# Optimization experiments

Measured on AMD Instinct MI355X. Metric: run time of the kernel, lower is better.

## Reference

```python
import math
import jax, jax.numpy as jnp
import numpy as np

L, H, D, FF, V, S = 12, 12, 768, 3072, 32000, 1024
HD = D // H
EPS = 1e-5
B, T = 2, 1024


def layernorm(x, w, b):
    mu = jnp.mean(x, axis=-1, keepdims=True)
    var = jnp.mean(jnp.square(x - mu), axis=-1, keepdims=True)
    return (x - mu) * jax.lax.rsqrt(var + EPS) * w + b


def setup_inputs() -> dict:
    key = jax.random.key(0)
    ks = jax.random.split(key, 12)
    std = 0.02
    std_res = 0.02 / math.sqrt(2 * L)  # out_proj / down_proj scaled init
    return {
        "input_ids": jax.random.randint(ks[0], (B, T), 0, V),
        "tok_emb": jax.random.normal(ks[1], (V, D), jnp.float32) * std,
        "pos_emb": jax.random.normal(ks[2], (S, D), jnp.float32) * std,
        "ln1_w": jnp.ones((L, D), jnp.float32),
        "ln1_b": jnp.zeros((L, D), jnp.float32),
        "qkv_w": jax.random.normal(ks[3], (L, 3 * D, D), jnp.float32) * std,
        "out_w": jax.random.normal(ks[4], (L, D, D), jnp.float32) * std_res,
        "ln2_w": jnp.ones((L, D), jnp.float32),
        "ln2_b": jnp.zeros((L, D), jnp.float32),
        "up_w": jax.random.normal(ks[5], (L, FF, D), jnp.float32) * std,
        "down_w": jax.random.normal(ks[6], (L, D, FF), jnp.float32) * std_res,
        "lnf_w": jnp.ones((D,), jnp.float32),
        "lnf_b": jnp.zeros((D,), jnp.float32),
    }


def reference(input_ids, tok_emb, pos_emb, ln1_w, ln1_b, qkv_w, out_w,
              ln2_w, ln2_b, up_w, down_w, lnf_w, lnf_b):
    b, t = input_ids.shape
    x = tok_emb[input_ids] + pos_emb[:t]  # (B,T,D); dropout = eval no-op
    causal = jnp.tril(jnp.ones((t, t), bool))  # (T,T)
    scale = 1.0 / math.sqrt(HD)

    def block(x, p):
        l1w, l1b, qkvw, ow, l2w, l2b, uw, dw = p
        h = layernorm(x, l1w, l1b)
        qkv = h @ qkvw.T  # (B,T,3D)
        q, k, v = jnp.split(qkv, 3, axis=-1)
        q = q.reshape(b, t, H, HD)
        k = k.reshape(b, t, H, HD)
        v = v.reshape(b, t, H, HD)
        scores = jnp.einsum('bihd,bjhd->bhij', q, k) * scale
        scores = jnp.where(causal, scores, -jnp.inf)
        probs = jax.nn.softmax(scores, axis=-1)  # attn_dropout = eval no-op
        o = jnp.einsum('bhij,bjhd->bihd', probs, v).reshape(b, t, D)
        x = x + o @ ow.T
        h2 = layernorm(x, l2w, l2b)
        x = x + jax.nn.gelu(h2 @ uw.T, approximate=False) @ dw.T
        return x, None

    x, _ = jax.lax.scan(block, x, (ln1_w, ln1_b, qkv_w, out_w, ln2_w, ln2_b, up_w, down_w))
    x = layernorm(x, lnf_w, lnf_b)
    logits = x @ tok_emb.T  # tied lm_head
    return logits
```

## Files before the change

### kernel.cpp

```cpp
#include <hip/hip_runtime.h>
#include <hip/hip_bf16.h>
#include <math.h>

#define L_  12
#define H_  12
#define D_  768
#define FF_ 3072
#define V_  32000
#define T_  1024
#define B_  2
#define BT_ (B_*T_)

typedef unsigned short ushort_t;
typedef unsigned int   uint_t;
typedef __bf16 bf16x8 __attribute__((ext_vector_type(8)));
typedef float  f32x4  __attribute__((ext_vector_type(4)));

__device__ __forceinline__ uint_t f2bf1(float f) {
    uint_t u = __builtin_bit_cast(uint_t, f);
    return (u + 0x7FFFu + ((u >> 16) & 1u)) >> 16;
}
__device__ __forceinline__ uint_t f2bf2(float lo, float hi) {
    return f2bf1(lo) | (f2bf1(hi) << 16);
}

__device__ __forceinline__ void gl_lds16(const ushort_t* g, ushort_t* l) {
    __builtin_amdgcn_global_load_lds(
        (const __attribute__((address_space(1))) uint_t*)g,
        (__attribute__((address_space(3))) uint_t*)l, 16, 0, 0);
}

__global__ __launch_bounds__(256) void cast_bf16(const float* __restrict__ in,
                                                 ushort_t* __restrict__ out, int n8)
{
    for (int i = blockIdx.x * 256 + threadIdx.x; i < n8; i += gridDim.x * 256) {
        const float4* p = (const float4*)(in + (size_t)i * 8);
        float4 a = p[0], b = p[1];
        *(uint4*)(out + (size_t)i * 8) =
            make_uint4(f2bf2(a.x,a.y), f2bf2(a.z,a.w), f2bf2(b.x,b.y), f2bf2(b.z,b.w));
    }
}

__global__ __launch_bounds__(256) void cast_layer(const float* __restrict__ q,
    const float* __restrict__ o, const float* __restrict__ u, const float* __restrict__ d,
    ushort_t* __restrict__ out)
{
    const int N0 = 3*D_*D_/8, N1 = N0 + D_*D_/8, N2 = N1 + FF_*D_/8, N3 = N2 + D_*FF_/8;
    for (int i = blockIdx.x * 256 + threadIdx.x; i < N3; i += gridDim.x * 256) {
        const float* src;
        if      (i < N0) src = q + (size_t)i * 8;
        else if (i < N1) src = o + (size_t)(i - N0) * 8;
        else if (i < N2) src = u + (size_t)(i - N1) * 8;
        else             src = d + (size_t)(i - N2) * 8;
        const float4* p = (const float4*)src;
        float4 a = p[0], b = p[1];
        *(uint4*)(out + (size_t)i * 8) =
            make_uint4(f2bf2(a.x,a.y), f2bf2(a.z,a.w), f2bf2(b.x,b.y), f2bf2(b.z,b.w));
    }
}

#define EPI_F32   0
#define EPI_BF16  1
#define EPI_GELU  2
#define EPI_PART  3
#define EPI_QKV   4

template <int EPI, int BM, int KS>
__global__ __launch_bounds__(256) void gemm_bt(
    const ushort_t* __restrict__ A, const ushort_t* __restrict__ W,
    const float* R, void* Cv, ushort_t* __restrict__ Vt, int N, int K, int Kc)
{
    constexpr int MI = BM / 32;
    constexpr int AH = BM * 32;
    constexpr int BH = 128 * 32;
    __shared__ ushort_t As[2 * AH];
    __shared__ ushort_t Bs[2 * BH];

    const int tid  = threadIdx.x;
    const int w    = tid >> 6;
    const int lane = tid & 63;

    const int nwg = gridDim.x;
    int swz = (blockIdx.x & 7) * (nwg >> 3) + (blockIdx.x >> 3);
    constexpr int MT = 2048 / BM;
    const int mt = swz & (MT - 1);
    int rest     = swz / MT;
    const int ks = rest & (KS - 1);
    const int nt = rest / KS;
    const int m0 = mt * BM, n0 = nt * 128;
    const int kb = ks * Kc;

    const int srow = lane >> 2;
    const int scol = ((lane & 3) ^ ((srow >> 1) & 3)) * 8;
    const ushort_t* gA = A + (size_t)(m0 + w * (BM / 4) + srow) * K + scol;
    const ushort_t* gW = W + (size_t)(n0 + w * 32 + srow) * K + scol;
    const size_t row16 = (size_t)16 * K;

    const int lr = lane & 15;
    const int lg = lane >> 4;
    const int wm = (w >> 1) * (BM / 2);
    const int wn = (w & 1) * 64;

    f32x4 acc[MI][4] = {};

    auto stage = [&](int buf, int k0) {
        ushort_t* lA = As + buf * AH + w * (BM / 4) * 32;
        ushort_t* lB = Bs + buf * BH + w * 1024;
        #pragma unroll
        for (int i = 0; i < BM / 64; ++i)
            gl_lds16(gA + k0 + i * row16, lA + i * 512);
        #pragma unroll
        for (int i = 0; i < 2; ++i)
            gl_lds16(gW + k0 + i * row16, lB + i * 512);
    };

    stage(0, kb);
    __syncthreads();
    int cur = 0;
    for (int k0 = kb; k0 < kb + Kc; k0 += 32) {
        if (k0 + 32 < kb + Kc) stage(cur ^ 1, k0 + 32);
        const ushort_t* Ab = As + cur * AH;
        const ushort_t* Bb = Bs + cur * BH;
        __builtin_amdgcn_s_setprio(1);
        {
            bf16x8 av[MI], bv[4];
            #pragma unroll
            for (int i = 0; i < MI; ++i) {
                int rr = wm + i * 16 + lr;
                int ch = lg ^ ((rr >> 1) & 3);
                av[i] = *(const bf16x8*)&Ab[rr * 32 + ch * 8];
            }
            #pragma unroll
            for (int j = 0; j < 4; ++j) {
                int rr = wn + j * 16 + lr;
                int ch = lg ^ ((rr >> 1) & 3);
                bv[j] = *(const bf16x8*)&Bb[rr * 32 + ch * 8];
            }
            #pragma unroll
            for (int i = 0; i < MI; ++i)
                #pragma unroll
                for (int j = 0; j < 4; ++j)
                    acc[i][j] = __builtin_amdgcn_mfma_f32_16x16x32_bf16(av[i], bv[j], acc[i][j], 0, 0, 0);
        }
        __builtin_amdgcn_s_setprio(0);
        __syncthreads();
        cur ^= 1;
    }

    float*    Cf = (float*)Cv;
    ushort_t* Cb = (ushort_t*)Cv;
    float*    Pp = (EPI == EPI_PART) ? (const_cast<float*>(R) + (size_t)ks * BT_ * D_) : nullptr;
    const int rbase = lg * 4;
    #pragma unroll
    for (int i = 0; i < MI; ++i) {
        #pragma unroll
        for (int j = 0; j < 4; ++j) {
            const int row0 = m0 + wm + i * 16 + rbase;
            const int col  = n0 + wn + j * 16 + lr;
            if (EPI == EPI_QKV) {
                if (col < 1536) {
                    #pragma unroll
                    for (int r = 0; r < 4; ++r)
                        Cb[(size_t)(row0 + r) * 2304 + col] = (ushort_t)f2bf1(acc[i][j][r]);
                } else {
                    const int hh = (col - 1536) >> 6, dd = (col - 1536) & 63;
                    const int bb = row0 >> 10,        tt = row0 & 1023;
                    uint2 pk;
                    pk.x = f2bf2(acc[i][j][0], acc[i][j][1]);
                    pk.y = f2bf2(acc[i][j][2], acc[i][j][3]);
                    *(uint2*)&Vt[(((size_t)bb * H_ + hh) * 64 + dd) * T_ + tt] = pk;
                }
            } else {
                #pragma unroll
                for (int r = 0; r < 4; ++r) {
                    size_t idx = (size_t)(row0 + r) * N + col;
                    float v = acc[i][j][r];
                    if (EPI == EPI_F32)  Cf[idx] = v;
                    if (EPI == EPI_BF16) Cb[idx] = (ushort_t)f2bf1(v);
                    if (EPI == EPI_GELU) Cb[idx] = (ushort_t)f2bf1(0.5f * v * (1.0f + erff(v * 0.70710678118654752f)));
                    if (EPI == EPI_PART) Pp[idx] = v;
                }
            }
        }
    }
}

__global__ __launch_bounds__(512, 2) void gemm256(
    const ushort_t* __restrict__ A, const ushort_t* __restrict__ W,
    float* __restrict__ C, int N, int K)
{
    __shared__ ushort_t Ls[2][2][256 * 64];

    const int tid  = threadIdx.x;
    const int w    = tid >> 6;
    const int lane = tid & 63;

    const int nwg = gridDim.x;
    int swz = (blockIdx.x & 7) * (nwg >> 3) + (blockIdx.x >> 3);
    const int mt = swz & 7;
    const int nt = swz >> 3;
    const int m0 = mt * 256, n0 = nt * 256;

    const int trow = tid >> 3;
    const int tchk = (tid & 7) ^ (trow & 7);
    const ushort_t* gA = A + (size_t)(m0 + trow) * K + tchk * 8;
    const ushort_t* gW = W + (size_t)(n0 + trow) * K + tchk * 8;

    const int lr = lane & 15;
    const int lg = lane >> 4;
    const int wm = (w >> 2) * 128;
    const int wn = (w & 3) * 64;

    f32x4 acc[8][4] = {};

    auto stage = [&](int buf, int k0) {
        #pragma unroll
        for (int seg = 0; seg < 4; ++seg) {
            gl_lds16(gA + (size_t)(seg * 64) * K + k0, &Ls[buf][0][seg * 4096 + w * 512]);
            gl_lds16(gW + (size_t)(seg * 64) * K + k0, &Ls[buf][1][seg * 4096 + w * 512]);
        }
    };

    stage(0, 0);
    __syncthreads();
    int cur = 0;
    const int NT = K / 64;
    for (int t = 0; t < NT; ++t) {
        if (t + 1 < NT) stage(cur ^ 1, (t + 1) * 64);
        const ushort_t* Ab = Ls[cur][0];
        const ushort_t* Bb = Ls[cur][1];
        bf16x8 bv[4][2];
        #pragma unroll
        for (int nf = 0; nf < 4; ++nf) {
            int rr = wn + nf * 16 + lr;
            #pragma unroll
            for (int kk = 0; kk < 2; ++kk) {
                int ch = (kk * 4 + lg) ^ (rr & 7);
                bv[nf][kk] = *(const bf16x8*)&Bb[rr * 64 + ch * 8];
            }
        }
        __builtin_amdgcn_s_setprio(1);
        #pragma unroll
        for (int mf = 0; mf < 8; ++mf) {
            int rr = wm + mf * 16 + lr;
            int ch0 = lg ^ (rr & 7);
            int ch1 = (4 + lg) ^ (rr & 7);
            bf16x8 a0 = *(const bf16x8*)&Ab[rr * 64 + ch0 * 8];
            bf16x8 a1 = *(const bf16x8*)&Ab[rr * 64 + ch1 * 8];
            #pragma unroll
            for (int nf = 0; nf < 4; ++nf) {
                acc[mf][nf] = __builtin_amdgcn_mfma_f32_16x16x32_bf16(a0, bv[nf][0], acc[mf][nf], 0, 0, 0);
                acc[mf][nf] = __builtin_amdgcn_mfma_f32_16x16x32_bf16(a1, bv[nf][1], acc[mf][nf], 0, 0, 0);
            }
        }
        __builtin_amdgcn_s_setprio(0);
        __syncthreads();
        cur ^= 1;
    }

    const int rbase = lg * 4;
    #pragma unroll
    for (int mf = 0; mf < 8; ++mf) {
        #pragma unroll
        for (int nf = 0; nf < 4; ++nf) {
            #pragma unroll
            for (int r = 0; r < 4; ++r) {
                int row = m0 + wm + mf * 16 + rbase + r;
                int col = n0 + wn + nf * 16 + lr;
                C[(size_t)row * N + col] = acc[mf][nf][r];
            }
        }
    }
}

__global__ __launch_bounds__(64) void attn_mfma(const ushort_t* __restrict__ qkv,
    const ushort_t* __restrict__ vt, ushort_t* __restrict__ o)
{
    __shared__ ushort_t Ps[16 * 136];

    int swz = (blockIdx.x & 7) * 192 + (blockIdx.x >> 3);
    const int bh  = swz >> 6;
    const int qtl = 63 - (swz & 63);
    const int b   = bh / H_;
    const int h   = bh % H_;
    const int lane = threadIdx.x;
    const int l15  = lane & 15;
    const int lg   = lane >> 4;
    const int qbase = qtl * 16;
    const int qlast = qbase + 15;

    const ushort_t* qp = qkv + ((size_t)(b * T_) + qbase + l15) * 2304 + h * 64 + lg * 8;
    bf16x8 qf0 = *(const bf16x8*)qp;
    bf16x8 qf1 = *(const bf16x8*)(qp + 32);

    f32x4 od[4] = {};
    float mr[4] = {-INFINITY, -INFINITY, -INFINITY, -INFINITY};
    float lr[4] = {0.f, 0.f, 0.f, 0.f};

    const ushort_t* kbase = qkv + (size_t)(b * T_) * 2304 + 768 + h * 64;
    const ushort_t* vbase = vt + (size_t)bh * 64 * T_;
    const float SC = 0.18033688011112042f;

    for (int j0 = 0; j0 <= qlast; j0 += 128) {
        f32x4 s[8];
        __builtin_amdgcn_s_setprio(1);
        #pragma unroll
        for (int n = 0; n < 8; ++n) {
            if (j0 + 16 * n <= qlast) {
                const ushort_t* kr = kbase + (size_t)(j0 + 16 * n + l15) * 2304 + lg * 8;
                bf16x8 kf0 = *(const bf16x8*)kr;
                bf16x8 kf1 = *(const bf16x8*)(kr + 32);
                f32x4 a = {};
                a = __builtin_amdgcn_mfma_f32_16x16x32_bf16(qf0, kf0, a, 0, 0, 0);
                a = __builtin_amdgcn_mfma_f32_16x16x32_bf16(qf1, kf1, a, 0, 0, 0);
                s[n] = a;
            } else {
                s[n] = f32x4{-INFINITY, -INFINITY, -INFINITY, -INFINITY};
            }
        }
        __builtin_amdgcn_s_setprio(0);

        #pragma unroll
        for (int n = 0; n < 8; ++n) {
            #pragma unroll
            for (int r = 0; r < 4; ++r) {
                float v = s[n][r] * SC;
                int jg = j0 + 16 * n + l15;
                int qg = qbase + lg * 4 + r;
                if (jg > qg) v = -INFINITY;
                s[n][r] = v;
            }
        }

        float al[4];
        #pragma unroll
        for (int r = 0; r < 4; ++r) {
            float tm = fmaxf(fmaxf(fmaxf(s[0][r], s[1][r]), fmaxf(s[2][r], s[3][r])),
                             fmaxf(fmaxf(s[4][r], s[5][r]), fmaxf(s[6][r], s[7][r])));
            tm = fmaxf(tm, __shfl_xor(tm, 1, 64));
            tm = fmaxf(tm, __shfl_xor(tm, 2, 64));
            tm = fmaxf(tm, __shfl_xor(tm, 4, 64));
            tm = fmaxf(tm, __shfl_xor(tm, 8, 64));
            float mn = fmaxf(mr[r], tm);
            al[r] = exp2f(mr[r] - mn);
            mr[r] = mn;
        }
        #pragma unroll
        for (int n = 0; n < 8; ++n)
            #pragma unroll
            for (int r = 0; r < 4; ++r)
                s[n][r] = exp2f(s[n][r] - mr[r]);
        #pragma unroll
        for (int r = 0; r < 4; ++r) {
            float ps = (s[0][r] + s[1][r]) + (s[2][r] + s[3][r]);
            ps += (s[4][r] + s[5][r]) + (s[6][r] + s[7][r]);
            ps += __shfl_xor(ps, 1, 64);
            ps += __shfl_xor(ps, 2, 64);
            ps += __shfl_xor(ps, 4, 64);
            ps += __shfl_xor(ps, 8, 64);
            lr[r] = lr[r] * al[r] + ps;
        }
        #pragma unroll
        for (int n = 0; n < 4; ++n)
            #pragma unroll
            for (int r = 0; r < 4; ++r)
                od[n][r] *= al[r];

        #pragma unroll
        for (int n = 0; n < 8; ++n)
            #pragma unroll
            for (int r = 0; r < 4; ++r)
                Ps[(lg * 4 + r) * 136 + 16 * n + l15] = (ushort_t)f2bf1(s[n][r]);

        __builtin_amdgcn_s_setprio(1);
        #pragma unroll
        for (int kc = 0; kc < 4; ++kc) {
            if (j0 + kc * 32 <= qlast) {
                bf16x8 pa = *(const bf16x8*)&Ps[l15 * 136 + kc * 32 + lg * 8];
                #pragma unroll
                for (int nn = 0; nn < 4; ++nn) {
                    bf16x8 vf = *(const bf16x8*)&vbase[(size_t)(16 * nn + l15) * T_ + j0 + kc * 32 + lg * 8];
                    od[nn] = __builtin_amdgcn_mfma_f32_16x16x32_bf16(pa, vf, od[nn], 0, 0, 0);
                }
            }
        }
        __builtin_amdgcn_s_setprio(0);
    }

    #pragma unroll
    for (int r = 0; r < 4; ++r) {
        float inv = 1.0f / lr[r];
        int row = qbase + lg * 4 + r;
        ushort_t* op = o + ((size_t)(b * T_ + row)) * 768 + h * 64 + l15;
        #pragma unroll
        for (int nn = 0; nn < 4; ++nn)
            op[16 * nn] = (ushort_t)f2bf1(od[nn][r] * inv);
    }
}

__device__ __forceinline__ void ln_body(float v0, float v1, float v2,
    const float* __restrict__ w, const float* __restrict__ bia,
    ushort_t* __restrict__ orow, int tid)
{
    float s  = v0 + v1 + v2;
    float s2 = v0 * v0 + v1 * v1 + v2 * v2;
    #pragma unroll
    for (int off = 32; off > 0; off >>= 1) {
        s  += __shfl_down(s,  off, 64);
        s2 += __shfl_down(s2, off, 64);
    }
    __shared__ float sh[8];
    const int wave = tid >> 6;
    if ((tid & 63) == 0) { sh[wave] = s; sh[4 + wave] = s2; }
    __syncthreads();
    float S  = sh[0] + sh[1] + sh[2] + sh[3];
    float S2 = sh[4] + sh[5] + sh[6] + sh[7];
    float mean = S * (1.f / 768.f);
    float var  = S2 * (1.f / 768.f) - mean * mean;
    float inv  = rsqrtf(var + 1e-5f);
    orow[tid]       = (ushort_t)f2bf1((v0 - mean) * inv * w[tid]       + bia[tid]);
    orow[tid + 256] = (ushort_t)f2bf1((v1 - mean) * inv * w[tid + 256] + bia[tid + 256]);
    orow[tid + 512] = (ushort_t)f2bf1((v2 - mean) * inv * w[tid + 512] + bia[tid + 512]);
}

__global__ __launch_bounds__(256) void ln_red4(float* __restrict__ x,
    const float* __restrict__ P, const float* __restrict__ w,
    const float* __restrict__ bia, ushort_t* __restrict__ out)
{
    const int row = blockIdx.x;
    const int tid = threadIdx.x;
    const size_t base = (size_t)row * 768;
    const size_t st = (size_t)BT_ * D_;
    float v0 = x[base + tid];
    float v1 = x[base + tid + 256];
    float v2 = x[base + tid + 512];
    #pragma unroll
    for (int p = 0; p < 4; ++p) {
        v0 += P[p * st + base + tid];
        v1 += P[p * st + base + tid + 256];
        v2 += P[p * st + base + tid + 512];
    }
    x[base + tid]       = v0;
    x[base + tid + 256] = v1;
    x[base + tid + 512] = v2;
    ln_body(v0, v1, v2, w, bia, out + base, tid);
}

__global__ __launch_bounds__(256) void embed_ln(const int* __restrict__ ids,
    const float* __restrict__ tok, const float* __restrict__ pos,
    const float* __restrict__ w, const float* __restrict__ bia,
    float* __restrict__ x, ushort_t* __restrict__ out)
{
    const int bt = blockIdx.x;
    const int t  = bt % T_;
    const int id = ids[bt];
    const int tid = threadIdx.x;
    const float* tr = tok + (size_t)id * 768;
    const float* pr = pos + (size_t)t * 768;
    const size_t base = (size_t)bt * 768;
    float v0 = tr[tid]       + pr[tid];
    float v1 = tr[tid + 256] + pr[tid + 256];
    float v2 = tr[tid + 512] + pr[tid + 512];
    x[base + tid]       = v0;
    x[base + tid + 256] = v1;
    x[base + tid + 512] = v2;
    ln_body(v0, v1, v2, w, bia, out + base, tid);
}

extern "C" void kernel_launch(void* const* d_in, const int* in_sizes, int n_in,
                              void* d_out, int out_size, void* d_ws, size_t ws_size,
                              hipStream_t stream)
{
    const int*   ids   = (const int*)  d_in[0];
    const float* tok   = (const float*)d_in[1];
    const float* pos   = (const float*)d_in[2];
    const float* ln1w  = (const float*)d_in[3];
    const float* ln1b  = (const float*)d_in[4];
    const float* qkvw  = (const float*)d_in[5];
    const float* outw  = (const float*)d_in[6];
    const float* ln2w  = (const float*)d_in[7];
    const float* ln2b  = (const float*)d_in[8];
    const float* upw   = (const float*)d_in[9];
    const float* downw = (const float*)d_in[10];
    const float* lnfw  = (const float*)d_in[11];
    const float* lnfb  = (const float*)d_in[12];
    float* out = (float*)d_out;

    char* ws = (char*)d_ws;
    ushort_t* h    = (ushort_t*)ws;
    float*    x    = (float*)   (ws + 3145728);
    ushort_t* qkv  = (ushort_t*)(ws + 9437184);
    ushort_t* o    = qkv  + (size_t)BT_ * 3 * D_;
    ushort_t* vt   = o    + (size_t)BT_ * D_;
    ushort_t* ffh  = vt   + (size_t)B_ * H_ * 64 * T_;
    ushort_t* layerW = (ushort_t*)(ws + 50331648);
    ushort_t* tokW   = (ushort_t*)(ws + 67108864);
    float*    P4     = (float*)(ws + 117440512);

    ushort_t* qkvwB  = layerW;
    ushort_t* outwB  = qkvwB + (size_t)3 * D_ * D_;
    ushort_t* upwB   = outwB + (size_t)D_ * D_;
    ushort_t* downwB = upwB  + (size_t)FF_ * D_;

    for (int l = 0; l < L_; ++l) {
        cast_layer<<<1024, 256, 0, stream>>>(
            qkvw  + (size_t)l * 3 * D_ * D_,
            outw  + (size_t)l * D_ * D_,
            upw   + (size_t)l * FF_ * D_,
            downw + (size_t)l * D_ * FF_, layerW);

        if (l == 0)
            embed_ln<<<BT_, 256, 0, stream>>>(ids, tok, pos, ln1w, ln1b, x, h);
        else
            ln_red4<<<BT_, 256, 0, stream>>>(x, P4, ln1w + l * D_, ln1b + l * D_, h);

        gemm_bt<EPI_QKV, 64, 1><<<32 * (3 * D_ / 128), 256, 0, stream>>>(
            h, qkvwB, nullptr, qkv, vt, 3 * D_, D_, D_);

        attn_mfma<<<B_ * H_ * (T_ / 16), 64, 0, stream>>>(qkv, vt, o);

        gemm_bt<EPI_PART, 64, 4><<<32 * (D_ / 128) * 4, 256, 0, stream>>>(
            o, outwB, P4, nullptr, nullptr, D_, D_, D_ / 4);

        ln_red4<<<BT_, 256, 0, stream>>>(x, P4, ln2w + l * D_, ln2b + l * D_, h);

        gemm_bt<EPI_GELU, 64, 1><<<32 * (FF_ / 128), 256, 0, stream>>>(
            h, upwB, nullptr, ffh, nullptr, FF_, D_, D_);

        gemm_bt<EPI_PART, 64, 4><<<32 * (D_ / 128) * 4, 256, 0, stream>>>(
            ffh, downwB, P4, nullptr, nullptr, D_, FF_, FF_ / 4);
    }

    ln_red4<<<BT_, 256, 0, stream>>>(x, P4, lnfw, lnfb, h);

    cast_bf16<<<2048, 256, 0, stream>>>(tok, tokW, V_ * D_ / 8);
    gemm256<<<(2048 / 256) * (V_ / 256), 512, 0, stream>>>(h, tokW, out, V_, D_);
}
```

Before: 1.977 ms.

## Cast all layer weights upfront and store split-K partials in bf16

Replaces the per-layer fused weight-cast kernel with four large casts of all layers' weights at the start, cutting twelve small launches and letting GEMMs index into a persistent bf16 weight buffer. Split-K partial sums for out_proj and down_proj are now stored as bf16 instead of fp32, which halves partial-buffer write and read traffic in the GEMM epilogue and the ln_red4 reduction. The cost is a larger workspace footprint and reduced precision of the residual partial sums before accumulation.

```diff
diff --git a/kernel.cpp b/kernel.cpp
--- a/kernel.cpp
+++ b/kernel.cpp
@@ -23,6 +23,9 @@
 __device__ __forceinline__ uint_t f2bf2(float lo, float hi) {
     return f2bf1(lo) | (f2bf1(hi) << 16);
 }
+__device__ __forceinline__ float bf2f(ushort_t u) {
+    return __builtin_bit_cast(float, (uint_t)u << 16);
+}
 
 __device__ __forceinline__ void gl_lds16(const ushort_t* g, ushort_t* l) {
     __builtin_amdgcn_global_load_lds(
@@ -35,24 +38,6 @@
 {
     for (int i = blockIdx.x * 256 + threadIdx.x; i < n8; i += gridDim.x * 256) {
         const float4* p = (const float4*)(in + (size_t)i * 8);
-        float4 a = p[0], b = p[1];
-        *(uint4*)(out + (size_t)i * 8) =
-            make_uint4(f2bf2(a.x,a.y), f2bf2(a.z,a.w), f2bf2(b.x,b.y), f2bf2(b.z,b.w));
-    }
-}
-
-__global__ __launch_bounds__(256) void cast_layer(const float* __restrict__ q,
-    const float* __restrict__ o, const float* __restrict__ u, const float* __restrict__ d,
-    ushort_t* __restrict__ out)
-{
-    const int N0 = 3*D_*D_/8, N1 = N0 + D_*D_/8, N2 = N1 + FF_*D_/8, N3 = N2 + D_*FF_/8;
-    for (int i = blockIdx.x * 256 + threadIdx.x; i < N3; i += gridDim.x * 256) {
-        const float* src;
-        if      (i < N0) src = q + (size_t)i * 8;
-        else if (i < N1) src = o + (size_t)(i - N0) * 8;
-        else if (i < N2) src = u + (size_t)(i - N1) * 8;
-        else             src = d + (size_t)(i - N2) * 8;
-        const float4* p = (const float4*)src;
         float4 a = p[0], b = p[1];
         *(uint4*)(out + (size_t)i * 8) =
             make_uint4(f2bf2(a.x,a.y), f2bf2(a.z,a.w), f2bf2(b.x,b.y), f2bf2(b.z,b.w));
@@ -149,7 +134,7 @@
 
     float*    Cf = (float*)Cv;
     ushort_t* Cb = (ushort_t*)Cv;
-    float*    Pp = (EPI == EPI_PART) ? (const_cast<float*>(R) + (size_t)ks * BT_ * D_) : nullptr;
+    ushort_t* Pp = (EPI == EPI_PART) ? ((ushort_t*)Cv + (size_t)ks * BT_ * D_) : nullptr;
     const int rbase = lg * 4;
     #pragma unroll
     for (int i = 0; i < MI; ++i) {
@@ -178,7 +163,7 @@
                     if (EPI == EPI_F32)  Cf[idx] = v;
                     if (EPI == EPI_BF16) Cb[idx] = (ushort_t)f2bf1(v);
                     if (EPI == EPI_GELU) Cb[idx] = (ushort_t)f2bf1(0.5f * v * (1.0f + erff(v * 0.70710678118654752f)));
-                    if (EPI == EPI_PART) Pp[idx] = v;
+                    if (EPI == EPI_PART) Pp[idx] = (ushort_t)f2bf1(v);
                 }
             }
         }
@@ -424,7 +409,7 @@
 }
 
 __global__ __launch_bounds__(256) void ln_red4(float* __restrict__ x,
-    const float* __restrict__ P, const float* __restrict__ w,
+    const ushort_t* __restrict__ P, const float* __restrict__ w,
     const float* __restrict__ bia, ushort_t* __restrict__ out)
 {
     const int row = blockIdx.x;
@@ -436,9 +421,9 @@
     float v2 = x[base + tid + 512];
     #pragma unroll
     for (int p = 0; p < 4; ++p) {
-        v0 += P[p * st + base + tid];
-        v1 += P[p * st + base + tid + 256];
-        v2 += P[p * st + base + tid + 512];
+        v0 += bf2f(P[p * st + base + tid]);
+        v1 += bf2f(P[p * st + base + tid + 256]);
+        v2 += bf2f(P[p * st + base + tid + 512]);
     }
     x[base + tid]       = v0;
     x[base + tid + 256] = v1;
@@ -493,42 +478,39 @@
     ushort_t* o    = qkv  + (size_t)BT_ * 3 * D_;
     ushort_t* vt   = o    + (size_t)BT_ * D_;
     ushort_t* ffh  = vt   + (size_t)B_ * H_ * 64 * T_;
-    ushort_t* layerW = (ushort_t*)(ws + 50331648);
-    ushort_t* tokW   = (ushort_t*)(ws + 67108864);
-    float*    P4     = (float*)(ws + 117440512);
-
-    ushort_t* qkvwB  = layerW;
-    ushort_t* outwB  = qkvwB + (size_t)3 * D_ * D_;
-    ushort_t* upwB   = outwB + (size_t)D_ * D_;
-    ushort_t* downwB = upwB  + (size_t)FF_ * D_;
+    ushort_t* P4   = (ushort_t*)(ws + 37748736);
+    ushort_t* tokW = (ushort_t*)(ws + 67108864);
+    ushort_t* qkvwB  = (ushort_t*)(ws + 117440512);
+    ushort_t* outwB  = qkvwB  + (size_t)L_ * 3 * D_ * D_;
+    ushort_t* upwB   = outwB  + (size_t)L_ * D_ * D_;
+    ushort_t* downwB = upwB   + (size_t)L_ * FF_ * D_;
+
+    cast_bf16<<<2048, 256, 0, stream>>>(qkvw,  qkvwB,  L_ * 3 * D_ * D_ / 8);
+    cast_bf16<<<2048, 256, 0, stream>>>(outw,  outwB,  L_ * D_ * D_ / 8);
+    cast_bf16<<<2048, 256, 0, stream>>>(upw,   upwB,   L_ * FF_ * D_ / 8);
+    cast_bf16<<<2048, 256, 0, stream>>>(downw, downwB, L_ * D_ * FF_ / 8);
 
     for (int l = 0; l < L_; ++l) {
-        cast_layer<<<1024, 256, 0, stream>>>(
-            qkvw  + (size_t)l * 3 * D_ * D_,
-            outw  + (size_t)l * D_ * D_,
-            upw   + (size_t)l * FF_ * D_,
-            downw + (size_t)l * D_ * FF_, layerW);
-
         if (l == 0)
             embed_ln<<<BT_, 256, 0, stream>>>(ids, tok, pos, ln1w, ln1b, x, h);
         else
             ln_red4<<<BT_, 256, 0, stream>>>(x, P4, ln1w + l * D_, ln1b + l * D_, h);
 
         gemm_bt<EPI_QKV, 64, 1><<<32 * (3 * D_ / 128), 256, 0, stream>>>(
-            h, qkvwB, nullptr, qkv, vt, 3 * D_, D_, D_);
+            h, qkvwB + (size_t)l * 3 * D_ * D_, nullptr, qkv, vt, 3 * D_, D_, D_);
 
         attn_mfma<<<B_ * H_ * (T_ / 16), 64, 0, stream>>>(qkv, vt, o);
 
         gemm_bt<EPI_PART, 64, 4><<<32 * (D_ / 128) * 4, 256, 0, stream>>>(
-            o, outwB, P4, nullptr, nullptr, D_, D_, D_ / 4);
+            o, outwB + (size_t)l * D_ * D_, nullptr, P4, nullptr, D_, D_, D_ / 4);
 
         ln_red4<<<BT_, 256, 0, stream>>>(x, P4, ln2w + l * D_, ln2b + l * D_, h);
 
         gemm_bt<EPI_GELU, 64, 1><<<32 * (FF_ / 128), 256, 0, stream>>>(
-            h, upwB, nullptr, ffh, nullptr, FF_, D_, D_);
+            h, upwB + (size_t)l * FF_ * D_, nullptr, ffh, nullptr, FF_, D_, D_);
 
         gemm_bt<EPI_PART, 64, 4><<<32 * (D_ / 128) * 4, 256, 0, stream>>>(
-            ffh, downwB, P4, nullptr, nullptr, D_, FF_, FF_ / 4);
+            ffh, downwB + (size_t)l * D_ * FF_, nullptr, P4, nullptr, D_, FF_, FF_ / 4);
     }
 
     ln_red4<<<BT_, 256, 0, stream>>>(x, P4, lnfw, lnfb, h);
```

Measured after the change: 2.042 ms. +3.3%, slower.
